# Kernel tuning notes

Hardware: AMD Instinct MI355X
Metric: run time of the kernel (lower is better)

## Reference

```python
import jax, jax.numpy as jnp
import numpy as np

B, S, D, H, OUT = 64, 512, 128, 2, 8
TD, VD, AD = 300, 35, 74
DH = D // H
EPS = 1e-5


def _layernorm(x, g, b):
    m = jnp.mean(x, -1, keepdims=True)
    v = jnp.var(x, -1, keepdims=True)
    return (x - m) * jax.lax.rsqrt(v + EPS) * g + b


def _attn_neg(q_in, k_in, v_in, Wq, bq, Wk, bk, Wv, bv, Wd, bd, g, beta):
    # MultiheadAttention2: probs = 1 - softmax(scores). dropout off (eval).
    b_, s_, _ = q_in.shape
    q = (q_in @ Wq + bq).reshape(b_, s_, H, DH).transpose(0, 2, 1, 3)
    k = (k_in @ Wk + bk).reshape(b_, k_in.shape[1], H, DH).transpose(0, 2, 1, 3)
    v = (v_in @ Wv + bv).reshape(b_, v_in.shape[1], H, DH).transpose(0, 2, 1, 3)
    scores = jnp.einsum('bhqd,bhkd->bhqk', q, k) / jnp.sqrt(jnp.float32(DH))
    probs = 1.0 - jax.nn.softmax(scores, axis=-1)
    ctx = jnp.einsum('bhqk,bhkd->bhqd', probs, v)
    ctx = ctx.transpose(0, 2, 1, 3).reshape(b_, s_, D)
    return _layernorm(ctx @ Wd + bd, g, beta)


def _gru_dir(x, Wih, Whh, bih, bhh):
    # torch GRU, gate order (r, z, n). x: [B,S,D] -> [B,S,H=128]
    gx = x @ Wih.T + bih  # [B,S,3H]
    gx_t = gx.transpose(1, 0, 2)  # [S,B,3H]

    def step(h, g_t):
        gh = h @ Whh.T + bhh
        xr, xz, xn = jnp.split(g_t, 3, -1)
        hr, hz, hn = jnp.split(gh, 3, -1)
        r = jax.nn.sigmoid(xr + hr)
        z = jax.nn.sigmoid(xz + hz)
        n = jnp.tanh(xn + r * hn)
        h_new = (1.0 - z) * n + z * h
        return h_new, h_new

    h0 = jnp.zeros((x.shape[0], D), x.dtype)
    _, hs = jax.lax.scan(step, h0, gx_t)
    return hs.transpose(1, 0, 2)


def _bigru(x, Wih, Whh, bih, bhh):
    fwd = _gru_dir(x, Wih[0], Whh[0], bih[0], bhh[0])
    bwd = _gru_dir(x[:, ::-1], Wih[1], Whh[1], bih[1], bhh[1])[:, ::-1]
    return jnp.concatenate([fwd, bwd], -1)


def setup_inputs() -> dict:
    key = jax.random.key(0)
    ks = iter(jax.random.split(key, 40))
    sc = 0.05

    def rn(shape, s=sc):
        return jax.random.normal(next(ks), shape, jnp.float32) * s

    inp = {
        'text_features': rn((B, S, TD), 1.0),
        'visual_features': rn((B, S, VD), 1.0),
        'audio_features': rn((B, S, AD), 1.0),
        'fc1W': rn((TD, D)), 'fc1b': rn((D,)),
        'fc2W': rn((VD, D)), 'fc2b': rn((D,)),
        'fc3W': rn((AD, D)), 'fc3b': rn((D,)),
        # 6 attention units: [ta_a, ta_b, tv_a, tv_b, va_a, va_b]
        'Wq': rn((6, D, D)), 'bq': rn((6, D)),
        'Wk': rn((6, D, D)), 'bk': rn((6, D)),
        'Wv': rn((6, D, D)), 'bv': rn((6, D)),
        'Wd': rn((6, D, D)), 'bd': rn((6, D)),
        'ln_g': jnp.ones((6, D), jnp.float32), 'ln_b': jnp.zeros((6, D), jnp.float32),
        # 3 bidirectional GRUs: [gru1(text), gru2(visual), gru3(audio)] x [fwd, bwd]
        'gWih': rn((3, 2, 3 * D, D)), 'gWhh': rn((3, 2, 3 * D, D)),
        'gbih': rn((3, 2, 3 * D)), 'gbhh': rn((3, 2, 3 * D)),
        # head: Linear(3D,2D) -> BN(eval) -> ReLU6 -> Linear(2D,out)
        'fW1': rn((3 * D, 2 * D)), 'fb1': rn((2 * D,)),
        'bn_g': jnp.ones((2 * D,), jnp.float32), 'bn_b': jnp.zeros((2 * D,), jnp.float32),
        'fW2': rn((2 * D, OUT)), 'fb2': rn((OUT,)),
    }
    return inp


def reference(text_features, visual_features, audio_features,
              fc1W, fc1b, fc2W, fc2b, fc3W, fc3b,
              Wq, bq, Wk, bk, Wv, bv, Wd, bd, ln_g, ln_b,
              gWih, gWhh, gbih, gbhh,
              fW1, fb1, bn_g, bn_b, fW2, fb2):
    t = text_features @ fc1W + fc1b
    v = visual_features @ fc2W + fc2b
    a = audio_features @ fc3W + fc3b

    def A(i, q, k, val):
        return _attn_neg(q, k, val, Wq[i], bq[i], Wk[i], bk[i], Wv[i], bv[i],
                         Wd[i], bd[i], ln_g[i], ln_b[i])

    # CrossAttention(a,b): b_out = a_attn(a,b,b); a_out = b_attn(b,a,a)
    audio_out1 = A(0, t, a, a)   # text_audio.a_attention
    text_out1 = A(1, a, t, t)    # text_audio.b_attention
    visual_out1 = A(2, t, v, v)  # text_visual.a_attention
    text_out2 = A(3, v, t, t)    # text_visual.b_attention
    audio_out2 = A(4, v, a, a)   # visual_audio.a_attention
    visual_out2 = A(5, a, v, v)  # visual_audio.b_attention

    text_out = (text_out1 + text_out2) / 2
    visual_out = (visual_out1 + visual_out2) / 2
    audio_out = (audio_out1 + audio_out2) / 2

    text_out = _bigru(text_out, gWih[0], gWhh[0], gbih[0], gbhh[0])
    visual_out = _bigru(visual_out, gWih[1], gWhh[1], gbih[1], gbhh[1])
    audio_out = _bigru(audio_out, gWih[2], gWhh[2], gbih[2], gbhh[2])

    out = jnp.concatenate([text_out, visual_out, audio_out], -1)  # [B,S,6D]
    out = jnp.mean((out[:, :, 3 * D:] + out[:, :, :3 * D]) / 2, axis=1)  # [B,3D]

    h = out @ fW1 + fb1
    # BatchNorm1d in eval with running stats (mean=0, var=1)
    h = h * jax.lax.rsqrt(jnp.float32(1.0 + EPS)) * bn_g + bn_b
    h = jnp.clip(h, 0.0, 6.0)  # ReLU6
    return h @ fW2 + fb2
```

## Files before the change

kernel.cpp:

```cpp
#include <hip/hip_runtime.h>
#include <hip/hip_bf16.h>

#define BB 64
#define SS 512
#define DD 128
#define NROW (BB * SS)
#define SZ ((size_t)NROW * DD)

#define LOG2E 1.4426950408889634f
#define QSCALE (0.125f * LOG2E)

typedef __attribute__((ext_vector_type(8))) short short8;
typedef __attribute__((ext_vector_type(4))) float f32x4;

#define WB_P1 0
#define WB_P2 40960
#define WB_P3 49152
#define WB_QKVD 61440
#define WB_WIH 454656
#define WB_WHH 749568
#define WB_TOTAL 1044480

__device__ __forceinline__ float frcp_(float x) { return __builtin_amdgcn_rcpf(x); }
__device__ __forceinline__ float fexp2_(float x) { return __builtin_amdgcn_exp2f(x); }
__device__ __forceinline__ float b2f(unsigned short u) {
  union { unsigned int i; float f; } x; x.i = ((unsigned int)u) << 16; return x.f;
}
__device__ __forceinline__ unsigned short f2b(float f) {
  __hip_bfloat16 b = __float2bfloat16(f);
  return *reinterpret_cast<unsigned short*>(&b);
}
__device__ __forceinline__ unsigned short f2b_trunc(float f) {
  union { float f; unsigned int i; } x; x.f = f; return (unsigned short)(x.i >> 16);
}

__global__ __launch_bounds__(256) void prep_kernel(
    const float* __restrict__ fc1W, const float* __restrict__ fc2W,
    const float* __restrict__ fc3W, const float* __restrict__ Wq,
    const float* __restrict__ Wk, const float* __restrict__ Wv,
    const float* __restrict__ Wd, const float* __restrict__ gWih,
    const float* __restrict__ gWhh, const float* __restrict__ gbih,
    const float* __restrict__ gbhh, const float* __restrict__ bq,
    unsigned short* __restrict__ WB, float* __restrict__ gbihs,
    float* __restrict__ bqs) {
  for (int idx = blockIdx.x * 256 + threadIdx.x; idx < WB_TOTAL;
       idx += gridDim.x * 256) {
    float v;
    if (idx < WB_P2) {
      int n = idx / 320, k = idx % 320;
      v = (k < 300) ? fc1W[k * 128 + n] : 0.f;
    } else if (idx < WB_P3) {
      int r = idx - WB_P2; int n = r >> 6, k = r & 63;
      v = (k < 35) ? fc2W[k * 128 + n] : 0.f;
    } else if (idx < WB_QKVD) {
      int r = idx - WB_P3; int n = r / 96, k = r % 96;
      v = (k < 74) ? fc3W[k * 128 + n] : 0.f;
    } else if (idx < WB_WIH) {
      int r = idx - WB_QKVD;
      int op = r / 98304; int r2 = r % 98304;
      int u = r2 >> 14; int r3 = r2 & 16383;
      int n = r3 >> 7, k = r3 & 127;
      const float* src = (op == 0) ? Wq : (op == 1) ? Wk : (op == 2) ? Wv : Wd;
      v = src[u * 16384 + k * 128 + n];
      if (op == 0) v *= QSCALE;
    } else if (idx < WB_WHH) {
      int r = idx - WB_WIH;
      int r3 = r % 49152;
      int gate = (r3 >> 7) >> 7;
      v = gWih[r] * (gate < 2 ? LOG2E : 2.f * LOG2E);
    } else {
      int r = idx - WB_WHH;
      int r3 = r % 49152;
      int gate = (r3 >> 7) >> 7;
      v = gWhh[r] * (gate < 2 ? LOG2E : 2.f * LOG2E);
    }
    WB[idx] = f2b(v);
  }
  for (int idx = blockIdx.x * 256 + threadIdx.x; idx < 6 * 384;
       idx += gridDim.x * 256) {
    int gate = (idx % 384) >> 7;
    float v = gbih[idx] + (gate < 2 ? gbhh[idx] : 0.f);
    gbihs[idx] = v * (gate < 2 ? LOG2E : 2.f * LOG2E);
  }
  for (int idx = blockIdx.x * 256 + threadIdx.x; idx < 6 * 128;
       idx += gridDim.x * 256) {
    bqs[idx] = bq[idx] * QSCALE;
  }
}

struct GArg {
  const void* A; const unsigned short* W; const float* bias; void* C;
  int Ka, Kp, abf, cbf, cs; float* vsum;
  const float* g2; const float* b2;
};
struct GArgs { GArg g[18]; int gw; int pad_; };

#define CST 5120

__global__ __launch_bounds__(256) void gemm_proj(GArgs args) {
  const GArg ga = args.g[blockIdx.z];
  __shared__ unsigned short As[3 * CST];
  __shared__ unsigned short Ws[3 * CST];
  const int t = threadIdx.x;
  const int lane = t & 63, q = lane >> 4, lm = lane & 15;
  const int w = t >> 6, wm = w >> 1, wn = w & 1;
  const int m0 = blockIdx.x * 128;
  const int row = t >> 1, half = t & 1;

  f32x4 acc[4][4];
#pragma unroll
  for (int i = 0; i < 4; ++i)
#pragma unroll
    for (int j = 0; j < 4; ++j) acc[i][j] = (f32x4){0.f, 0.f, 0.f, 0.f};

  const float* Ab = (const float*)ga.A + (size_t)(m0 + row) * ga.Ka;
  const unsigned short* Wb = ga.W + (size_t)row * ga.Kp;

  for (int k0 = 0; k0 < ga.Kp; k0 += 96) {
    const int SW = (ga.Kp - k0 < 96) ? (ga.Kp - k0) : 96;
    const int hw = SW >> 1;
    const int cbase = half * hw;
    if (k0) __syncthreads();

    if (ga.abf) {
#pragma unroll 4
      for (int j = 0; j < hw; j += 4) {
        const int cg = k0 + cbase + j;
        float4 v = {0.f, 0.f, 0.f, 0.f};
        if (cg + 4 <= ga.Ka) v = *reinterpret_cast<const float4*>(Ab + cg);
        const int cc = cbase + j, lc = cc >> 5, co = cc & 31;
        unsigned short tp[4] = {f2b(v.x), f2b(v.y), f2b(v.z), f2b(v.w)};
        *reinterpret_cast<unsigned long long*>(&As[lc * CST + row * 40 + co]) =
            *reinterpret_cast<unsigned long long*>(tp);
      }
    } else {
#pragma unroll 4
      for (int j = 0; j < hw; j += 4) {
        const int cg = k0 + cbase + j;
        unsigned short tp[4];
#pragma unroll
        for (int e = 0; e < 4; ++e)
          tp[e] = (cg + e < ga.Ka) ? f2b(Ab[cg + e]) : (unsigned short)0;
        const int cc = cbase + j, lc = cc >> 5, co = cc & 31;
        *reinterpret_cast<unsigned long long*>(&As[lc * CST + row * 40 + co]) =
            *reinterpret_cast<unsigned long long*>(tp);
      }
    }
#pragma unroll 2
    for (int j = 0; j < hw; j += 8) {
      const int cg = k0 + cbase + j;
      short8 v = *reinterpret_cast<const short8*>(Wb + cg);
      const int cc = cbase + j, lc = cc >> 5, co = cc & 31;
      *reinterpret_cast<short8*>(&Ws[lc * CST + row * 40 + co]) = v;
    }
    __syncthreads();

    const int nc = SW >> 5;
    for (int c = 0; c < nc; ++c) {
      short8 af[4], bfv[4];
#pragma unroll
      for (int mi = 0; mi < 4; ++mi)
        af[mi] = *reinterpret_cast<const short8*>(
            &As[c * CST + (wm * 64 + mi * 16 + lm) * 40 + q * 8]);
#pragma unroll
      for (int ni = 0; ni < 4; ++ni)
        bfv[ni] = *reinterpret_cast<const short8*>(
            &Ws[c * CST + (wn * 64 + ni * 16 + lm) * 40 + q * 8]);
#pragma unroll
      for (int mi = 0; mi < 4; ++mi)
#pragma unroll
        for (int ni = 0; ni < 4; ++ni)
          acc[mi][ni] = __builtin_amdgcn_mfma_f32_16x16x32_bf16(
              af[mi], bfv[ni], acc[mi][ni], 0, 0, 0);
    }
  }

#pragma unroll
  for (int ni = 0; ni < 4; ++ni) {
    const int colg = wn * 64 + ni * 16 + lm;
    const float bv = ga.bias[colg];
#pragma unroll
    for (int mi = 0; mi < 4; ++mi) {
      const int rg = m0 + wm * 64 + mi * 16 + q * 4;
#pragma unroll
      for (int r = 0; r < 4; ++r) {
        float v = acc[mi][ni][r] + bv;
        ((unsigned short*)ga.C)[(size_t)(rg + r) * ga.cs + colg] = f2b(v);
      }
    }
  }
}

__global__ __launch_bounds__(256) void gemm_k128g(GArgs args) {
  const int base = blockIdx.z * args.gw;
  const int nw = args.g[base].abf;
  __shared__ unsigned short As4[4 * CST];
  __shared__ unsigned short Ws4[4 * CST];
  const int t = threadIdx.x;
  const int lane = t & 63, q = lane >> 4, lm = lane & 15;
  const int w = t >> 6, wm = w >> 1, wn = w & 1;
  const int m0 = blockIdx.x * 128;

  const int srow = t >> 4, scol = (t & 15) * 8;
  const int sc = scol >> 5, soff = scol & 31;

  {
    const unsigned short* Ab =
        (const unsigned short*)args.g[base].A + (size_t)(m0 + srow) * 128 + scol;
#pragma unroll
    for (int p = 0; p < 8; ++p) {
      short8 av = *reinterpret_cast<const short8*>(Ab + (size_t)p * 16 * 128);
      *reinterpret_cast<short8*>(&As4[sc * CST + (srow + p * 16) * 40 + soff]) = av;
    }
  }

  for (int i = 0; i < nw; ++i) {
    const GArg ge = args.g[base + i];
    if (i) __syncthreads();
    {
      const unsigned short* Wg = ge.W + (size_t)srow * 128 + scol;
#pragma unroll
      for (int p = 0; p < 8; ++p) {
        short8 wv = *reinterpret_cast<const short8*>(Wg + (size_t)p * 16 * 128);
        *reinterpret_cast<short8*>(&Ws4[sc * CST + (srow + p * 16) * 40 + soff]) = wv;
      }
    }
    __syncthreads();

    f32x4 acc[4][4];
#pragma unroll
    for (int ii = 0; ii < 4; ++ii)
#pragma unroll
      for (int jj = 0; jj < 4; ++jj) acc[ii][jj] = (f32x4){0.f, 0.f, 0.f, 0.f};

#pragma unroll
    for (int c = 0; c < 4; ++c) {
      short8 af[4], bfv[4];
#pragma unroll
      for (int mi = 0; mi < 4; ++mi)
        af[mi] = *reinterpret_cast<const short8*>(
            &As4[c * CST + (wm * 64 + mi * 16 + lm) * 40 + q * 8]);
#pragma unroll
      for (int ni = 0; ni < 4; ++ni)
        bfv[ni] = *reinterpret_cast<const short8*>(
            &Ws4[c * CST + (wn * 64 + ni * 16 + lm) * 40 + q * 8]);
#pragma unroll
      for (int mi = 0; mi < 4; ++mi)
#pragma unroll
        for (int ni = 0; ni < 4; ++ni)
          acc[mi][ni] = __builtin_amdgcn_mfma_f32_16x16x32_bf16(
              af[mi], bfv[ni], acc[mi][ni], 0, 0, 0);
    }

#pragma unroll
    for (int ni = 0; ni < 4; ++ni) {
      const int colg = wn * 64 + ni * 16 + lm;
      const float bv = ge.bias[colg];
#pragma unroll
      for (int mi = 0; mi < 4; ++mi) {
        const int rg = m0 + wm * 64 + mi * 16 + q * 4;
#pragma unroll
        for (int r = 0; r < 4; ++r) {
          float v = acc[mi][ni][r] + bv;
          ((unsigned short*)ge.C)[(size_t)(rg + r) * ge.cs + colg] = f2b(v);
        }
      }
    }
    if (ge.vsum) {
      float* vp = ge.vsum + (size_t)(m0 >> 9) * 128;
#pragma unroll
      for (int ni = 0; ni < 4; ++ni) {
        const int colg = wn * 64 + ni * 16 + lm;
        float s = 16.f * ge.bias[colg];
#pragma unroll
        for (int mi = 0; mi < 4; ++mi)
#pragma unroll
          for (int r = 0; r < 4; ++r) s += acc[mi][ni][r];
        atomicAdd(&vp[colg], s);
      }
    }
  }
}

__global__ __launch_bounds__(256) void gemm_dln2(GArgs args) {
  const GArg g1 = args.g[blockIdx.z * 2];
  const GArg g2e = args.g[blockIdx.z * 2 + 1];
  __shared__ unsigned short As4[4 * CST];
  __shared__ unsigned short Ws4[4 * CST];
  const int t = threadIdx.x;
  const int lane = t & 63, q = lane >> 4, lm = lane & 15;
  const int w = t >> 6, wm = w >> 1, wn = w & 1;
  const int m0 = blockIdx.x * 128;

  const int srow = t >> 4, scol = (t & 15) * 8;
  const int sc = scol >> 5, soff = scol & 31;

  f32x4 acc1[4][4], acc2[4][4];
#pragma unroll
  for (int i = 0; i < 4; ++i)
#pragma unroll
    for (int j = 0; j < 4; ++j) {
      acc1[i][j] = (f32x4){0.f, 0.f, 0.f, 0.f};
      acc2[i][j] = (f32x4){0.f, 0.f, 0.f, 0.f};
    }

#pragma unroll
  for (int pass = 0; pass < 2; ++pass) {
    const GArg& ge = pass ? g2e : g1;
    if (pass) __syncthreads();
    {
      const unsigned short* Ab =
          (const unsigned short*)ge.A + (size_t)(m0 + srow) * 128 + scol;
      const unsigned short* Wg = ge.W + (size_t)srow * 128 + scol;
#pragma unroll
      for (int p = 0; p < 8; ++p) {
        short8 av = *reinterpret_cast<const short8*>(Ab + (size_t)p * 16 * 128);
        short8 wv = *reinterpret_cast<const short8*>(Wg + (size_t)p * 16 * 128);
        *reinterpret_cast<short8*>(&As4[sc * CST + (srow + p * 16) * 40 + soff]) = av;
        *reinterpret_cast<short8*>(&Ws4[sc * CST + (srow + p * 16) * 40 + soff]) = wv;
      }
    }
    __syncthreads();

#pragma unroll
    for (int c = 0; c < 4; ++c) {
      short8 af[4], bfv[4];
#pragma unroll
      for (int mi = 0; mi < 4; ++mi)
        af[mi] = *reinterpret_cast<const short8*>(
            &As4[c * CST + (wm * 64 + mi * 16 + lm) * 40 + q * 8]);
#pragma unroll
      for (int ni = 0; ni < 4; ++ni)
        bfv[ni] = *reinterpret_cast<const short8*>(
            &Ws4[c * CST + (wn * 64 + ni * 16 + lm) * 40 + q * 8]);
#pragma unroll
      for (int mi = 0; mi < 4; ++mi)
#pragma unroll
        for (int ni = 0; ni < 4; ++ni) {
          if (pass == 0)
            acc1[mi][ni] = __builtin_amdgcn_mfma_f32_16x16x32_bf16(
                af[mi], bfv[ni], acc1[mi][ni], 0, 0, 0);
          else
            acc2[mi][ni] = __builtin_amdgcn_mfma_f32_16x16x32_bf16(
                af[mi], bfv[ni], acc2[mi][ni], 0, 0, 0);
        }
    }
  }

  float bv1[4], gg1[4], bb1[4], bv2[4], gg2[4], bb2[4];
#pragma unroll
  for (int ni = 0; ni < 4; ++ni) {
    const int colg = wn * 64 + ni * 16 + lm;
    bv1[ni] = g1.bias[colg]; gg1[ni] = g1.g2[colg]; bb1[ni] = g1.b2[colg];
    bv2[ni] = g2e.bias[colg]; gg2[ni] = g2e.g2[colg]; bb2[ni] = g2e.b2[colg];
  }
  float s1[4][4], q1[4][4], s2[4][4], q2[4][4];
#pragma unroll
  for (int mi = 0; mi < 4; ++mi)
#pragma unroll
    for (int r = 0; r < 4; ++r) {
      float a1 = 0.f, c1 = 0.f, a2 = 0.f, c2 = 0.f;
#pragma unroll
      for (int ni = 0; ni < 4; ++ni) {
        float v1 = acc1[mi][ni][r] + bv1[ni];
        float v2 = acc2[mi][ni][r] + bv2[ni];
        a1 += v1; c1 += v1 * v1;
        a2 += v2; c2 += v2 * v2;
      }
      s1[mi][r] = a1; q1[mi][r] = c1; s2[mi][r] = a2; q2[mi][r] = c2;
    }
#pragma unroll
  for (int m = 1; m < 16; m <<= 1)
#pragma unroll
    for (int mi = 0; mi < 4; ++mi)
#pragma unroll
      for (int r = 0; r < 4; ++r) {
        s1[mi][r] += __shfl_xor(s1[mi][r], m);
        q1[mi][r] += __shfl_xor(q1[mi][r], m);
        s2[mi][r] += __shfl_xor(s2[mi][r], m);
        q2[mi][r] += __shfl_xor(q2[mi][r], m);
      }
  float4* LB = reinterpret_cast<float4*>(As4);
  __syncthreads();
  if (lm == 0) {
#pragma unroll
    for (int mi = 0; mi < 4; ++mi)
#pragma unroll
      for (int r = 0; r < 4; ++r) {
        float4 p;
        p.x = s1[mi][r]; p.y = q1[mi][r]; p.z = s2[mi][r]; p.w = q2[mi][r];
        LB[(wm * 64 + mi * 16 + q * 4 + r) * 2 + wn] = p;
      }
  }
  __syncthreads();

#pragma unroll
  for (int mi = 0; mi < 4; ++mi)
#pragma unroll
    for (int r = 0; r < 4; ++r) {
      float4 oth = LB[(wm * 64 + mi * 16 + q * 4 + r) * 2 + (wn ^ 1)];
      const float m1 = (s1[mi][r] + oth.x) * (1.f / 128.f);
      const float va1 = (q1[mi][r] + oth.y) * (1.f / 128.f) - m1 * m1;
      const float rs1 = rsqrtf(va1 + 1e-5f);
      const float m2 = (s2[mi][r] + oth.z) * (1.f / 128.f);
      const float va2 = (q2[mi][r] + oth.w) * (1.f / 128.f) - m2 * m2;
      const float rs2 = rsqrtf(va2 + 1e-5f);
      const int rg = m0 + wm * 64 + mi * 16 + q * 4 + r;
      unsigned short* cp = (unsigned short*)g1.C + (size_t)rg * 128;
#pragma unroll
      for (int ni = 0; ni < 4; ++ni) {
        const int colg = wn * 64 + ni * 16 + lm;
        float v1 = acc1[mi][ni][r] + bv1[ni];
        float v2 = acc2[mi][ni][r] + bv2[ni];
        float o = 0.5f * ((v1 - m1) * rs1 * gg1[ni] + bb1[ni]) +
                  0.5f * ((v2 - m2) * rs2 * gg2[ni] + bb2[ni]);
        cp[colg] = f2b(o);
      }
    }
}

__global__ __launch_bounds__(256) void attn2(
    const unsigned short* __restrict__ QKV, const float* __restrict__ VS,
    unsigned short* __restrict__ CTX) {
  __shared__ unsigned short Vt[64 * 72];
  __shared__ unsigned short Pt[4][16 * 72];
  const int t = threadIdx.x;
  const int w = t >> 6, lane = t & 63, quad = lane >> 4, lm = lane & 15;
  const int z = blockIdx.z;
  const int bh = blockIdx.y, b = bh >> 1, h = bh & 1;
  const int qbase = blockIdx.x * 256;

  const unsigned short* Qg = QKV + (size_t)(z * 3 + 0) * SZ;
  const unsigned short* Kg = QKV + (size_t)(z * 3 + 1) * SZ;
  const unsigned short* Vg = QKV + (size_t)(z * 3 + 2) * SZ;

  short8 aq[4][2];
#pragma unroll
  for (int qt = 0; qt < 4; ++qt)
#pragma unroll
    for (int c = 0; c < 2; ++c)
      aq[qt][c] = *reinterpret_cast<const short8*>(
          Qg + ((size_t)(b * SS + qbase + qt * 64 + w * 16 + lm)) * DD +
          h * 64 + c * 32 + quad * 8);

  const f32x4 czero = {0.f, 0.f, 0.f, 0.f};
  f32x4 o[4][4];
#pragma unroll
  for (int i = 0; i < 4; ++i)
#pragma unroll
    for (int j = 0; j < 4; ++j) o[i][j] = czero;
  float suml[4][4];
#pragma unroll
  for (int i = 0; i < 4; ++i)
#pragma unroll
    for (int j = 0; j < 4; ++j) suml[i][j] = 0.f;

  const int vk = t >> 3, vd0 = (t & 7) * 8;

  for (int kt = 0; kt < 8; ++kt) {
    const int k0 = kt * 64;
    __syncthreads();
#pragma unroll
    for (int i = 0; i < 2; ++i) {
      const int k = vk + i * 32;
      short8 vv = *reinterpret_cast<const short8*>(
          Vg + ((size_t)(b * SS + k0 + k)) * DD + h * 64 + vd0);
#pragma unroll
      for (int j = 0; j < 8; ++j) {
        const int d = vd0 + j;
        Vt[d * 72 + (k ^ (d & 56))] = (unsigned short)vv[j];
      }
    }
    __syncthreads();

    short8 bk[4][2];
#pragma unroll
    for (int nt = 0; nt < 4; ++nt)
#pragma unroll
      for (int c = 0; c < 2; ++c)
        bk[nt][c] = *reinterpret_cast<const short8*>(
            Kg + ((size_t)(b * SS + k0 + nt * 16 + lm)) * DD + h * 64 +
            c * 32 + quad * 8);
    short8 bvv[4][2];
#pragma unroll
    for (int dt = 0; dt < 4; ++dt) {
      const int d = dt * 16 + lm;
#pragma unroll
      for (int c = 0; c < 2; ++c)
        bvv[dt][c] = *reinterpret_cast<const short8*>(
            &Vt[d * 72 + ((c * 32 + quad * 8) ^ (d & 56))]);
    }

#pragma unroll
    for (int qt = 0; qt < 4; ++qt) {
      f32x4 sacc[4];
#pragma unroll
      for (int nt = 0; nt < 4; ++nt)
        sacc[nt] = __builtin_amdgcn_mfma_f32_16x16x32_bf16(
            aq[qt][0], bk[nt][0], czero, 0, 0, 0);
#pragma unroll
      for (int nt = 0; nt < 4; ++nt)
        sacc[nt] = __builtin_amdgcn_mfma_f32_16x16x32_bf16(
            aq[qt][1], bk[nt][1], sacc[nt], 0, 0, 0);
#pragma unroll
      for (int nt = 0; nt < 4; ++nt) {
#pragma unroll
        for (int r = 0; r < 4; ++r) {
          float p = fexp2_(sacc[nt][r]);
          suml[qt][r] += p;
          Pt[w][(quad * 4 + r) * 72 + nt * 16 + lm] = f2b_trunc(p);
        }
      }
#pragma unroll
      for (int c = 0; c < 2; ++c) {
        short8 ap = *reinterpret_cast<const short8*>(
            &Pt[w][lm * 72 + c * 32 + quad * 8]);
#pragma unroll
        for (int dt = 0; dt < 4; ++dt)
          o[qt][dt] = __builtin_amdgcn_mfma_f32_16x16x32_bf16(
              ap, bvv[dt][c], o[qt][dt], 0, 0, 0);
      }
    }
  }
#pragma unroll
  for (int qt = 0; qt < 4; ++qt)
#pragma unroll
    for (int r = 0; r < 4; ++r) {
#pragma unroll
      for (int m = 1; m < 16; m <<= 1)
        suml[qt][r] += __shfl_xor(suml[qt][r], m);
    }
  const float* vsp = VS + (size_t)(z * BB + b) * DD + h * 64;
#pragma unroll
  for (int qt = 0; qt < 4; ++qt)
#pragma unroll
    for (int dt = 0; dt < 4; ++dt) {
      const int col = dt * 16 + lm;
      const float vs = vsp[col];
#pragma unroll
      for (int r = 0; r < 4; ++r) {
        const int row = qbase + qt * 64 + w * 16 + quad * 4 + r;
        CTX[(size_t)z * SZ + ((size_t)(b * SS + row)) * DD + h * 64 + col] =
            f2b(vs - o[qt][dt][r] * frcp_(suml[qt][r]));
      }
    }
}

#define AST 136

__global__ __launch_bounds__(512, 1) void gru8(
    const unsigned short* __restrict__ GXR, const unsigned short* __restrict__ WB,
    const float* __restrict__ gbhh, float* __restrict__ HS) {
  __shared__ unsigned short Abuf[2][16 * AST];
  const int rec = blockIdx.y, bg = blockIdx.x;
  const int dir = rec & 1;
  const int t = threadIdx.x;
  const int w = t >> 6, lane = t & 63, q = lane >> 4, lm = lane & 15;
  const int o = w * 16 + lm;
  const int b = bg * 4 + q;

  short8 Bh[3][4];
  const unsigned short* whh = WB + WB_WHH + (size_t)rec * 49152;
#pragma unroll
  for (int gate = 0; gate < 3; ++gate)
#pragma unroll
    for (int c = 0; c < 4; ++c)
      Bh[gate][c] = *reinterpret_cast<const short8*>(
          whh + (size_t)(gate * 128 + o) * 128 + c * 32 + q * 8);
  const float bhn = gbhh[rec * 384 + 256 + o] * (2.f * LOG2E);
  const f32x4 czero = {0.f, 0.f, 0.f, 0.f};
  const f32x4 cbhn = {bhn, 0.f, 0.f, 0.f};

  float h = 0.f, hsum = 0.f;
  for (int i = t; i < 2 * 16 * AST; i += 512)
    (&Abuf[0][0])[i] = 0;

  const unsigned short* gx0 = GXR + (size_t)rec * 12582912 +
      ((size_t)b * 512 + (dir ? 511 : 0)) * 384 + o;
  const ptrdiff_t st = dir ? -384 : 384;

  unsigned short ring[4][3];
#pragma unroll
  for (int pp = 0; pp < 4; ++pp) {
    const unsigned short* gp = gx0 + (ptrdiff_t)pp * st;
#pragma unroll
    for (int j = 0; j < 3; ++j) ring[pp][j] = gp[j * 128];
  }
  const unsigned short* pf = gx0 + (ptrdiff_t)4 * st;
  __syncthreads();

#pragma unroll 4
  for (int s = 0; s < SS; ++s) {
    const int p = s & 1, slot = s & 3;
    const float gxr = b2f(ring[slot][0]);
    const float gxz = b2f(ring[slot][1]);
    const float gxn = b2f(ring[slot][2]);
#pragma unroll
    for (int j = 0; j < 3; ++j) ring[slot][j] = pf[j * 128];
    pf += (s < SS - 5) ? st : 0;

    short8 ah0 = *reinterpret_cast<const short8*>(&Abuf[p][lm * AST + 0 + q * 8]);
    short8 ah1 = *reinterpret_cast<const short8*>(&Abuf[p][lm * AST + 32 + q * 8]);
    short8 ah2 = *reinterpret_cast<const short8*>(&Abuf[p][lm * AST + 64 + q * 8]);
    short8 ah3 = *reinterpret_cast<const short8*>(&Abuf[p][lm * AST + 96 + q * 8]);
    f32x4 r0 = __builtin_amdgcn_mfma_f32_16x16x32_bf16(ah0, Bh[0][0], czero, 0, 0, 0);
    f32x4 r1 = __builtin_amdgcn_mfma_f32_16x16x32_bf16(ah2, Bh[0][2], czero, 0, 0, 0);
    f32x4 z0 = __builtin_amdgcn_mfma_f32_16x16x32_bf16(ah0, Bh[1][0], czero, 0, 0, 0);
    f32x4 z1 = __builtin_amdgcn_mfma_f32_16x16x32_bf16(ah2, Bh[1][2], czero, 0, 0, 0);
    f32x4 n0 = __builtin_amdgcn_mfma_f32_16x16x32_bf16(ah0, Bh[2][0], cbhn, 0, 0, 0);
    f32x4 n1 = __builtin_amdgcn_mfma_f32_16x16x32_bf16(ah2, Bh[2][2], czero, 0, 0, 0);
    r0 = __builtin_amdgcn_mfma_f32_16x16x32_bf16(ah1, Bh[0][1], r0, 0, 0, 0);
    r1 = __builtin_amdgcn_mfma_f32_16x16x32_bf16(ah3, Bh[0][3], r1, 0, 0, 0);
    z0 = __builtin_amdgcn_mfma_f32_16x16x32_bf16(ah1, Bh[1][1], z0, 0, 0, 0);
    z1 = __builtin_amdgcn_mfma_f32_16x16x32_bf16(ah3, Bh[1][3], z1, 0, 0, 0);
    n0 = __builtin_amdgcn_mfma_f32_16x16x32_bf16(ah1, Bh[2][1], n0, 0, 0, 0);
    n1 = __builtin_amdgcn_mfma_f32_16x16x32_bf16(ah3, Bh[2][3], n1, 0, 0, 0);

    float rr = frcp_(1.f + fexp2_(-(gxr + r0[0] + r1[0])));
    float zz = frcp_(1.f + fexp2_(-(gxz + z0[0] + z1[0])));
    float nn = 1.f - 2.f * frcp_(fexp2_(gxn + rr * (n0[0] + n1[0])) + 1.f);
    h = nn + zz * (h - nn);
    hsum += h;
    Abuf[p ^ 1][(q * 4) * AST + o] = f2b_trunc(h);
    asm volatile("s_waitcnt lgkmcnt(0)\n\ts_barrier" ::: "memory");
  }
  HS[((size_t)rec * BB + bg * 4 + q) * 128 + o] = hsum;
}

__global__ __launch_bounds__(256) void head_kernel(
    const float* __restrict__ HS, const float* __restrict__ fW1,
    const float* __restrict__ fb1, const float* __restrict__ bng,
    const float* __restrict__ bnb, const float* __restrict__ fW2,
    const float* __restrict__ fb2, float* __restrict__ out) {
  __shared__ float pl[384];
  __shared__ float h1[256];
  int b = blockIdx.x, n = threadIdx.x;
  {
    int j = n;
    int seg = j >> 7, oo = j & 127;
    pl[j] = (HS[((size_t)seg * BB + b) * 128 + oo] +
             HS[((size_t)(seg + 3) * BB + b) * 128 + oo]) * (0.5f / 512.f);
  }
  if (n < 128) {
    int j = 256 + n;
    int seg = j >> 7, oo = j & 127;
    pl[j] = (HS[((size_t)seg * BB + b) * 128 + oo] +
             HS[((size_t)(seg + 3) * BB + b) * 128 + oo]) * (0.5f / 512.f);
  }
  __syncthreads();
  float acc = fb1[n];
  for (int k = 0; k < 384; ++k) acc += pl[k] * fW1[k * 256 + n];
  float hv = acc * rsqrtf(1.f + 1e-5f) * bng[n] + bnb[n];
  hv = fminf(fmaxf(hv, 0.f), 6.f);
  h1[n] = hv;
  __syncthreads();
  if (n < 8) {
    float a2 = fb2[n];
    for (int k = 0; k < 256; ++k) a2 += h1[k] * fW2[k * 8 + n];
    out[b * 8 + n] = a2;
  }
}

extern "C" void kernel_launch(void* const* d_in, const int* in_sizes, int n_in,
                              void* d_out, int out_size, void* d_ws,
                              size_t ws_size, hipStream_t stream) {
  (void)in_sizes; (void)n_in; (void)out_size; (void)ws_size;
  const float* text = (const float*)d_in[0];
  const float* vis  = (const float*)d_in[1];
  const float* aud  = (const float*)d_in[2];
  const float* fc1W = (const float*)d_in[3];
  const float* fc1b = (const float*)d_in[4];
  const float* fc2W = (const float*)d_in[5];
  const float* fc2b = (const float*)d_in[6];
  const float* fc3W = (const float*)d_in[7];
  const float* fc3b = (const float*)d_in[8];
  const float* Wq = (const float*)d_in[9];
  const float* bq = (const float*)d_in[10];
  const float* Wk = (const float*)d_in[11];
  const float* bk = (const float*)d_in[12];
  const float* Wv = (const float*)d_in[13];
  const float* bv = (const float*)d_in[14];
  const float* Wd = (const float*)d_in[15];
  const float* bd = (const float*)d_in[16];
  const float* lng = (const float*)d_in[17];
  const float* lnb = (const float*)d_in[18];
  const float* gWih = (const float*)d_in[19];
  const float* gWhh = (const float*)d_in[20];
  const float* gbih = (const float*)d_in[21];
  const float* gbhh = (const float*)d_in[22];
  const float* fW1 = (const float*)d_in[23];
  const float* fb1 = (const float*)d_in[24];
  const float* bng = (const float*)d_in[25];
  const float* bnb = (const float*)d_in[26];
  const float* fW2 = (const float*)d_in[27];
  const float* fb2 = (const float*)d_in[28];
  float* out = (float*)d_out;

  unsigned short* WSB = (unsigned short*)d_ws;
  unsigned short* T   = WSB;
  unsigned short* Vv  = WSB + SZ;
  unsigned short* Aa  = WSB + 2 * SZ;
  unsigned short* QKV = WSB + 3 * SZ;
  unsigned short* CTX = WSB + 12 * SZ;
  unsigned short* GXR = WSB;
  unsigned short* GRUIN = WSB + 18 * SZ;
  unsigned short* WB  = WSB + 21 * SZ;
  float* VS = (float*)(WSB + 21 * SZ + 1048576);
  float* HS = VS + 6 * 64 * 128;
  float* gbihs = HS + 6 * 64 * 128;
  float* bqs = gbihs + 6 * 384;

  prep_kernel<<<dim3(1024), dim3(256), 0, stream>>>(
      fc1W, fc2W, fc3W, Wq, Wk, Wv, Wd, gWih, gWhh, gbih, gbhh, bq, WB,
      gbihs, bqs);
  hipMemsetAsync(VS, 0, 6 * 64 * 128 * sizeof(float), stream);

  {
    GArgs ga{};
    ga.gw = 1;
    ga.g[0] = {text, WB + WB_P1, fc1b, T, 300, 320, 1, 1, 128};
    ga.g[1] = {vis,  WB + WB_P2, fc2b, Vv, 35, 64, 0, 1, 128};
    ga.g[2] = {aud,  WB + WB_P3, fc3b, Aa, 74, 96, 0, 1, 128};
    gemm_proj<<<dim3(256, 1, 3), dim3(256), 0, stream>>>(ga);
  }

  const int qsel[6] = {0, 2, 0, 1, 1, 2};
  const int ksel[6] = {2, 0, 1, 0, 2, 1};
  unsigned short* proj[3] = {T, Vv, Aa};

  for (int phase = 0; phase < 2; ++phase) {
    GArgs ga{};
    ga.gw = 4;
    int cnt[3] = {0, 0, 0};
    for (int ul = 0; ul < 3; ++ul) {
      int u = phase * 3 + ul;
      for (int op = 0; op < 3; ++op) {
        int a = (op == 0) ? qsel[u] : ksel[u];
        int z = ul * 3 + op;
        const float* bias = (op == 0) ? (bqs + u * 128)
                          : (op == 1) ? (bk + u * 128) : (bv + u * 128);
        float* vsum = (op == 2) ? (VS + (size_t)u * BB * DD) : nullptr;
        ga.g[a * 4 + cnt[a]] = {proj[a],
                                WB + WB_QKVD + op * 98304 + u * 16384, bias,
                                QKV + (size_t)z * SZ, 128, 128, 0, 1, 128,
                                vsum};
        cnt[a]++;
      }
    }
    for (int a = 0; a < 3; ++a) ga.g[a * 4].abf = cnt[a];
    gemm_k128g<<<dim3(256, 1, 3), dim3(256), 0, stream>>>(ga);
    attn2<<<dim3(2, 128, 3), dim3(256), 0, stream>>>(
        QKV, VS + phase * 3 * BB * DD, CTX + (size_t)phase * 3 * SZ);
  }

  {
    const int u1t[3] = {1, 2, 0};
    const int u2t[3] = {3, 5, 4};
    GArgs ga{};
    ga.gw = 2;
    for (int g = 0; g < 3; ++g) {
      int u1 = u1t[g], u2 = u2t[g];
      ga.g[g * 2 + 0] = {CTX + (size_t)u1 * SZ,
                         WB + WB_QKVD + 3 * 98304 + u1 * 16384,
                         bd + u1 * 128, GRUIN + (size_t)g * SZ, 128, 128, 2, 0,
                         128, nullptr, lng + u1 * 128, lnb + u1 * 128};
      ga.g[g * 2 + 1] = {CTX + (size_t)u2 * SZ,
                         WB + WB_QKVD + 3 * 98304 + u2 * 16384,
                         bd + u2 * 128, nullptr, 128, 128, 0, 0,
                         128, nullptr, lng + u2 * 128, lnb + u2 * 128};
    }
    gemm_dln2<<<dim3(256, 1, 3), dim3(256), 0, stream>>>(ga);
  }

  {
    GArgs ga{};
    ga.gw = 6;
    for (int g = 0; g < 3; ++g) {
      for (int i = 0; i < 6; ++i) {
        int dr = i / 3, ny = i % 3, r6 = g * 2 + dr;
        ga.g[g * 6 + i] = {GRUIN + (size_t)g * SZ,
                           WB + WB_WIH + r6 * 49152 + ny * 16384,
                           gbihs + r6 * 384 + ny * 128,
                           GXR + (size_t)r6 * 12582912 + ny * 128,
                           128, 128, (i == 0) ? 6 : 0, 1, 384, nullptr};
      }
    }
    gemm_k128g<<<dim3(256, 1, 3), dim3(256), 0, stream>>>(ga);
  }

  gru8<<<dim3(16, 6), dim3(512), 0, stream>>>(GXR, WB, gbhh, HS);
  head_kernel<<<dim3(BB), dim3(256), 0, stream>>>(HS, fW1, fb1, bng, bnb, fW2, fb2, out);
}
```

Baseline: 674.7 us.

## Fuse dense+layernorm with GRU input-projection GEMMs, dropping GRUIN round trip

The dense-projection plus dual-layernorm kernel now keeps its bf16 output tile in shared memory and immediately runs the six GRU input-gate GEMMs (both directions, r/z/n) on it, writing the gate pre-activations directly. This removes the intermediate GRUIN buffer write and reread and one kernel launch. Because GXR now overlaps CTX, which is still being read, the work is split into two launches and the last two recurrences' gate buffers are relocated, with gru8 updated to match. The cost is longer per-block serial work with fewer blocks in the second launch (only one z-slice), so load balance may suffer.

```diff
diff --git a/kernel.cpp b/kernel.cpp
--- a/kernel.cpp
+++ b/kernel.cpp
@@ -20,6 +20,9 @@
 #define WB_WIH 454656
 #define WB_WHH 749568
 #define WB_TOTAL 1044480
+
+#define GXR_OFF4 (13 * SZ)
+#define GXR_OFF5 (17 * SZ)
 
 __device__ __forceinline__ float frcp_(float x) { return __builtin_amdgcn_rcpf(x); }
 __device__ __forceinline__ float fexp2_(float x) { return __builtin_amdgcn_exp2f(x); }
@@ -93,7 +96,7 @@
   int Ka, Kp, abf, cbf, cs; float* vsum;
   const float* g2; const float* b2;
 };
-struct GArgs { GArg g[18]; int gw; int pad_; };
+struct GArgs { GArg g[24]; int gw; int pad_; };
 
 #define CST 5120
 
@@ -282,9 +285,10 @@
   }
 }
 
-__global__ __launch_bounds__(256) void gemm_dln2(GArgs args) {
-  const GArg g1 = args.g[blockIdx.z * 2];
-  const GArg g2e = args.g[blockIdx.z * 2 + 1];
+__global__ __launch_bounds__(256) void gemm_dlng(GArgs args) {
+  const int base = blockIdx.z * 8;
+  const GArg g1 = args.g[base];
+  const GArg g2e = args.g[base + 1];
   __shared__ unsigned short As4[4 * CST];
   __shared__ unsigned short Ws4[4 * CST];
   const int t = threadIdx.x;
@@ -405,18 +409,84 @@
       const float m2 = (s2[mi][r] + oth.z) * (1.f / 128.f);
       const float va2 = (q2[mi][r] + oth.w) * (1.f / 128.f) - m2 * m2;
       const float rs2 = rsqrtf(va2 + 1e-5f);
-      const int rg = m0 + wm * 64 + mi * 16 + q * 4 + r;
-      unsigned short* cp = (unsigned short*)g1.C + (size_t)rg * 128;
 #pragma unroll
       for (int ni = 0; ni < 4; ++ni) {
-        const int colg = wn * 64 + ni * 16 + lm;
         float v1 = acc1[mi][ni][r] + bv1[ni];
         float v2 = acc2[mi][ni][r] + bv2[ni];
-        float o = 0.5f * ((v1 - m1) * rs1 * gg1[ni] + bb1[ni]) +
-                  0.5f * ((v2 - m2) * rs2 * gg2[ni] + bb2[ni]);
-        cp[colg] = f2b(o);
-      }
-    }
+        acc1[mi][ni][r] = 0.5f * ((v1 - m1) * rs1 * gg1[ni] + bb1[ni]) +
+                          0.5f * ((v2 - m2) * rs2 * gg2[ni] + bb2[ni]);
+      }
+    }
+
+  __syncthreads();
+#pragma unroll
+  for (int mi = 0; mi < 4; ++mi) {
+#pragma unroll
+    for (int ni = 0; ni < 4; ++ni) {
+      const int col = wn * 64 + ni * 16 + lm;
+      const int cc = col >> 5, co = col & 31;
+#pragma unroll
+      for (int r = 0; r < 4; ++r) {
+        const int row = wm * 64 + mi * 16 + q * 4 + r;
+        As4[cc * CST + row * 40 + co] = f2b(acc1[mi][ni][r]);
+      }
+    }
+  }
+  __syncthreads();
+
+  for (int i = 0; i < 6; ++i) {
+    const GArg ge = args.g[base + 2 + i];
+    if (i) __syncthreads();
+    {
+      const unsigned short* Wg = ge.W + (size_t)srow * 128 + scol;
+#pragma unroll
+      for (int p = 0; p < 8; ++p) {
+        short8 wv = *reinterpret_cast<const short8*>(Wg + (size_t)p * 16 * 128);
+        *reinterpret_cast<short8*>(&Ws4[sc * CST + (srow + p * 16) * 40 + soff]) = wv;
+      }
+    }
+    __syncthreads();
+
+    f32x4 acc[4][4];
+#pragma unroll
+    for (int ii = 0; ii < 4; ++ii)
+#pragma unroll
+      for (int jj = 0; jj < 4; ++jj) acc[ii][jj] = (f32x4){0.f, 0.f, 0.f, 0.f};
+
+#pragma unroll
+    for (int c = 0; c < 4; ++c) {
+      short8 af[4], bfv[4];
+#pragma unroll
+      for (int mi = 0; mi < 4; ++mi)
+        af[mi] = *reinterpret_cast<const short8*>(
+            &As4[c * CST + (wm * 64 + mi * 16 + lm) * 40 + q * 8]);
+#pragma unroll
+      for (int ni = 0; ni < 4; ++ni)
+        bfv[ni] = *reinterpret_cast<const short8*>(
+            &Ws4[c * CST + (wn * 64 + ni * 16 + lm) * 40 + q * 8]);
+#pragma unroll
+      for (int mi = 0; mi < 4; ++mi)
+#pragma unroll
+        for (int ni = 0; ni < 4; ++ni)
+          acc[mi][ni] = __builtin_amdgcn_mfma_f32_16x16x32_bf16(
+              af[mi], bfv[ni], acc[mi][ni], 0, 0, 0);
+    }
+
+#pragma unroll
+    for (int ni = 0; ni < 4; ++ni) {
+      const int colg = wn * 64 + ni * 16 + lm;
+      const float bv = ge.bias[colg];
+#pragma unroll
+      for (int mi = 0; mi < 4; ++mi) {
+        const int rg = m0 + wm * 64 + mi * 16 + q * 4;
+#pragma unroll
+        for (int r = 0; r < 4; ++r) {
+          float v = acc[mi][ni][r] + bv;
+          ((unsigned short*)ge.C)[(size_t)(rg + r) * ge.cs + colg] = f2b(v);
+        }
+      }
+    }
+  }
 }
 
 __global__ __launch_bounds__(256) void attn2(
@@ -575,7 +645,9 @@
   for (int i = t; i < 2 * 16 * AST; i += 512)
     (&Abuf[0][0])[i] = 0;
 
-  const unsigned short* gx0 = GXR + (size_t)rec * 12582912 +
+  const size_t roff = (rec < 4) ? (size_t)rec * 12582912
+                                : (rec == 4 ? GXR_OFF4 : GXR_OFF5);
+  const unsigned short* gx0 = GXR + roff +
       ((size_t)b * 512 + (dir ? 511 : 0)) * 384 + o;
   const ptrdiff_t st = dir ? -384 : 384;
 
@@ -703,7 +775,6 @@
   unsigned short* QKV = WSB + 3 * SZ;
   unsigned short* CTX = WSB + 12 * SZ;
   unsigned short* GXR = WSB;
-  unsigned short* GRUIN = WSB + 18 * SZ;
   unsigned short* WB  = WSB + 21 * SZ;
   float* VS = (float*)(WSB + 21 * SZ + 1048576);
   float* HS = VS + 6 * 64 * 128;
@@ -756,36 +827,37 @@
   {
     const int u1t[3] = {1, 2, 0};
     const int u2t[3] = {3, 5, 4};
-    GArgs ga{};
-    ga.gw = 2;
-    for (int g = 0; g < 3; ++g) {
-      int u1 = u1t[g], u2 = u2t[g];
-      ga.g[g * 2 + 0] = {CTX + (size_t)u1 * SZ,
-                         WB + WB_QKVD + 3 * 98304 + u1 * 16384,
-                         bd + u1 * 128, GRUIN + (size_t)g * SZ, 128, 128, 2, 0,
-                         128, nullptr, lng + u1 * 128, lnb + u1 * 128};
-      ga.g[g * 2 + 1] = {CTX + (size_t)u2 * SZ,
-                         WB + WB_QKVD + 3 * 98304 + u2 * 16384,
-                         bd + u2 * 128, nullptr, 128, 128, 0, 0,
-                         128, nullptr, lng + u2 * 128, lnb + u2 * 128};
-    }
-    gemm_dln2<<<dim3(256, 1, 3), dim3(256), 0, stream>>>(ga);
-  }
-
-  {
-    GArgs ga{};
-    ga.gw = 6;
-    for (int g = 0; g < 3; ++g) {
-      for (int i = 0; i < 6; ++i) {
-        int dr = i / 3, ny = i % 3, r6 = g * 2 + dr;
-        ga.g[g * 6 + i] = {GRUIN + (size_t)g * SZ,
-                           WB + WB_WIH + r6 * 49152 + ny * 16384,
-                           gbihs + r6 * 384 + ny * 128,
-                           GXR + (size_t)r6 * 12582912 + ny * 128,
-                           128, 128, (i == 0) ? 6 : 0, 1, 384, nullptr};
-      }
-    }
-    gemm_k128g<<<dim3(256, 1, 3), dim3(256), 0, stream>>>(ga);
+    unsigned short* gxr_base[6];
+    for (int r6 = 0; r6 < 4; ++r6) gxr_base[r6] = WSB + (size_t)r6 * 12582912;
+    gxr_base[4] = WSB + GXR_OFF4;
+    gxr_base[5] = WSB + GXR_OFF5;
+
+    for (int launch = 0; launch < 2; ++launch) {
+      const int g0 = launch == 0 ? 0 : 2;
+      const int ng = launch == 0 ? 2 : 1;
+      GArgs ga{};
+      for (int gi = 0; gi < ng; ++gi) {
+        int g = g0 + gi;
+        int u1 = u1t[g], u2 = u2t[g];
+        ga.g[gi * 8 + 0] = {CTX + (size_t)u1 * SZ,
+                            WB + WB_QKVD + 3 * 98304 + u1 * 16384,
+                            bd + u1 * 128, nullptr, 128, 128, 0, 0,
+                            128, nullptr, lng + u1 * 128, lnb + u1 * 128};
+        ga.g[gi * 8 + 1] = {CTX + (size_t)u2 * SZ,
+                            WB + WB_QKVD + 3 * 98304 + u2 * 16384,
+                            bd + u2 * 128, nullptr, 128, 128, 0, 0,
+                            128, nullptr, lng + u2 * 128, lnb + u2 * 128};
+        for (int i = 0; i < 6; ++i) {
+          int dr = i / 3, ny = i % 3, r6 = g * 2 + dr;
+          ga.g[gi * 8 + 2 + i] = {nullptr,
+                                  WB + WB_WIH + r6 * 49152 + ny * 16384,
+                                  gbihs + r6 * 384 + ny * 128,
+                                  gxr_base[r6] + ny * 128,
+                                  128, 128, 0, 1, 384, nullptr};
+        }
+      }
+      gemm_dlng<<<dim3(256, 1, ng), dim3(256), 0, stream>>>(ga);
+    }
   }
 
   gru8<<<dim3(16, 6), dim3(512), 0, stream>>>(GXR, WB, gbhh, HS);
```

Measured after the change: 685.8 us. No clear change (+1.6%).
